# Kernel optimization log

Measured on AMD Instinct MI355X. Metric: run time of the kernel, lower is better.

The kernel has to match this reference:

```python
import jax, jax.numpy as jnp
import numpy as np

B, N, DIM, HEADS = 2, 1024, 1024, 16
HD = DIM // HEADS  # 64


def setup_inputs() -> dict:
    key = jax.random.key(0)
    ks = jax.random.split(key, 8)
    f = lambda k, s: jax.random.normal(k, s, dtype=jnp.float32)
    inv = np.float32(1.0 / np.sqrt(DIM))
    return {
        'x_real': f(ks[0], (B, N, DIM)),
        'x_imag': f(ks[1], (B, N, DIM)),
        'freqs_real': f(ks[2], (N, HD)),
        'freqs_imag': f(ks[3], (N, HD)),
        'Wqkv_r': f(ks[4], (3 * DIM, DIM)) * inv,
        'Wqkv_i': f(ks[5], (3 * DIM, DIM)) * inv,
        'bqkv_r': jnp.zeros((3 * DIM,), jnp.float32),
        'bqkv_i': jnp.zeros((3 * DIM,), jnp.float32),
        'Wout_r': f(ks[6], (DIM, DIM)) * inv,
        'Wout_i': f(ks[7], (DIM, DIM)) * inv,
        'bout_r': jnp.zeros((DIM,), jnp.float32),
        'bout_i': jnp.zeros((DIM,), jnp.float32),
    }


def reference(x_real, x_imag, freqs_real, freqs_imag,
              Wqkv_r, Wqkv_i, bqkv_r, bqkv_i,
              Wout_r, Wout_i, bout_r, bout_i):
    cplx = jax.lax.complex
    x = cplx(x_real, x_imag)                    # [b, n, d] complex64
    Wqkv = cplx(Wqkv_r, Wqkv_i)                 # [3d, d]
    bqkv = cplx(bqkv_r, bqkv_i)
    Wout = cplx(Wout_r, Wout_i)
    bout = cplx(bout_r, bout_i)
    freqs = cplx(freqs_real, freqs_imag)        # [n, hd]

    scale = HD ** (-0.5)

    # ComplexLinear: x @ W^T + b -> [b, n, 3d]
    qkv = jnp.einsum('bnd,ed->bne', x, Wqkv) + bqkv
    # rearrange 'b n (h d qkv) -> qkv b h n d' (qkv index fastest-varying)
    qkv = qkv.reshape(B, N, HEADS, HD, 3)
    q = jnp.transpose(qkv[..., 0], (0, 2, 1, 3))  # [b, h, n, hd]
    k = jnp.transpose(qkv[..., 1], (0, 2, 1, 3))
    v = jnp.transpose(qkv[..., 2], (0, 2, 1, 3))

    # complex rotary: elementwise multiply by freqs [n, hd]
    q = q * freqs
    k = k * freqs

    # complex QK^H -> [b, h, n, n]
    dots = jnp.einsum('bhnd,bhmd->bhnm', q, jnp.conj(k))
    attn = jax.nn.softmax(jnp.abs(dots) * scale, axis=-1)  # real float32

    # real attn @ complex v (promotes to complex64)
    out = jnp.einsum('bhnm,bhmd->bhnd', attn, v)
    out = jnp.transpose(out, (0, 2, 1, 3)).reshape(B, N, DIM)  # b n (h d)

    out = jnp.einsum('bnd,ed->bne', out, Wout) + bout
    # return real/imag stacked so baseline comparison is on real arrays
    return jnp.stack([jnp.real(out), jnp.imag(out)], axis=0)  # [2, b, n, d]
```

## Files before the change

### kernel.cpp

```cpp
#include <hip/hip_runtime.h>
#include <hip/hip_bf16.h>
#include <stdint.h>

#define B 2
#define N 1024
#define DIM 1024
#define HEADS 16
#define HD 64
#define E3 (3*DIM)
#define M (B*N)

typedef __hip_bfloat16 bf16;
typedef __attribute__((ext_vector_type(8))) short short8v;
typedef __attribute__((ext_vector_type(4))) float f32x4;
typedef __attribute__((ext_vector_type(4))) unsigned int u32x4;

__device__ __forceinline__ float scrub(float v) {
    return (v == v && fabsf(v) < 1e30f) ? v : 0.0f;
}
__device__ __forceinline__ float b2f(bf16 x) { return scrub(__bfloat162float(x)); }

template<bool FP32>
__device__ __forceinline__ float ldin(const void* p, int i) {
    if (FP32) return scrub(((const float*)p)[i]);
    else      return scrub(__bfloat162float(((const bf16*)p)[i]));
}

__device__ __forceinline__ bool sniff_fp32(const void* x, int tid, int* sbad) {
    if (tid == 0) *sbad = 0;
    __syncthreads();
    if (tid < 64) {
        const unsigned short* u = (const unsigned short*)x;
        int ex = (u[tid] >> 7) & 0xFF;
        if (ex == 0xFF || ex >= 135 || (ex != 0 && ex <= 118))
            atomicAdd(sbad, 1);
    }
    __syncthreads();
    return *sbad > 4;
}

__device__ __forceinline__ short f2bs(float x) {
    bf16 h = __float2bfloat16(x);
    return __builtin_bit_cast(short, h);
}
__device__ __forceinline__ short8v neg8(short8v x) {
    u32x4 u = __builtin_bit_cast(u32x4, x);
    u ^= 0x80008000u;
    return __builtin_bit_cast(short8v, u);
}
__device__ __forceinline__ f32x4 mfma16(short8v a, short8v b, f32x4 c) {
    return __builtin_amdgcn_mfma_f32_16x16x32_bf16(a, b, c, 0, 0, 0);
}

__device__ __forceinline__ void gload16(const bf16* g, bf16* l) {
    __builtin_amdgcn_global_load_lds(
        (const __attribute__((address_space(1))) void*)g,
        (__attribute__((address_space(3))) void*)l, 16, 0, 0);
}

__device__ __forceinline__ void cvt8(bf16* dhi, bf16* dlo, const float* s) {
    float4 a = *(const float4*)s;
    float4 b = *(const float4*)(s + 4);
    float v[8] = {a.x,a.y,a.z,a.w,b.x,b.y,b.z,b.w};
    short8v hi, lo;
    #pragma unroll
    for (int e = 0; e < 8; ++e) {
        float f = scrub(v[e]);
        bf16 h = __float2bfloat16(f);
        hi[e] = __builtin_bit_cast(short, h);
        lo[e] = f2bs(f - __bfloat162float(h));
    }
    *(short8v*)dhi = hi;
    *(short8v*)dlo = lo;
}
__device__ __forceinline__ void cvt8h(bf16* dhi, const float* s) {
    float4 a = *(const float4*)s;
    float4 b = *(const float4*)(s + 4);
    float v[8] = {a.x,a.y,a.z,a.w,b.x,b.y,b.z,b.w};
    short8v hi;
    #pragma unroll
    for (int e = 0; e < 8; ++e)
        hi[e] = f2bs(scrub(v[e]));
    *(short8v*)dhi = hi;
}

#define PLB 2048

__device__ __forceinline__ short8v frag_ldp(const bf16* base, int row, int j) {
    int p = row >> 1;
    int c = (((row & 1) << 2) | j) ^ (p & 7);
    return *(const short8v*)(base + p*64 + c*8);
}

template<bool ASPLIT, int BM, int NI>
__device__ __forceinline__ void cgemm_async(
    const bf16* Arh, const bf16* Aih, const bf16* Arl, const bf16* Ail,
    const bf16* Brh, const bf16* Bih,
    int row0, int col0,
    bf16* sA0, bf16* sA1, bf16* sB0, bf16* sB1,
    f32x4 (*accr)[NI], f32x4 (*accs)[NI], f32x4 (*acci)[NI])
{
    constexpr int PLA = BM*32;
    const int t  = threadIdx.x;
    const int w  = t >> 6, l = t & 63;
    const int lr = l & 15, lg = l >> 4;
    const int wm = (NI == 4) ? w : (w >> 1);
    const int wn = (NI == 4) ? 0 : (w & 1);

    const int pb  = t >> 3;
    const int cpb = (t & 7) ^ (pb & 7);
    const int srb = 2*pb + (cpb >> 2);
    const int sjb = cpb & 3;

    auto stage = [&](int buf, int k0) {
        bf16* dsA = buf ? sA1 : sA0;
        bf16* dsB = buf ? sB1 : sB0;
        #pragma unroll
        for (int u = 0; u < BM/64; ++u) {
            int c   = t + 256*u;
            int pa  = c >> 3;
            int cpa = (c & 7) ^ (pa & 7);
            int sra = 2*pa + (cpa >> 2);
            int sja = cpa & 3;
            size_t aoff = (size_t)(row0 + sra)*DIM + k0 + sja*8;
            gload16(Arh + aoff, dsA + c*8);
            gload16(Aih + aoff, dsA + PLA + c*8);
            if constexpr (ASPLIT) {
                gload16(Arl + aoff, dsA + 2*PLA + c*8);
                gload16(Ail + aoff, dsA + 3*PLA + c*8);
            }
        }
        size_t boff = (size_t)(col0 + srb)*DIM + k0 + sjb*8;
        gload16(Brh + boff, dsB + t*8);
        gload16(Bih + boff, dsB + PLB + t*8);
    };

    stage(0, 0);
    __syncthreads();
    int cur = 0;

    for (int k0 = 0; k0 < DIM; k0 += 32) {
        if (k0 + 32 < DIM) stage(cur ^ 1, k0 + 32);

        const bf16* sA = cur ? sA1 : sA0;
        const bf16* sB = cur ? sB1 : sB0;

        short8v arh[2], aih[2], arl[2], ail[2];
        #pragma unroll
        for (int mi = 0; mi < 2; ++mi) {
            int arow = wm*32 + mi*16 + lr;
            arh[mi] = frag_ldp(sA,       arow, lg);
            aih[mi] = frag_ldp(sA + PLA, arow, lg);
            if constexpr (ASPLIT) {
                arl[mi] = frag_ldp(sA + 2*PLA, arow, lg);
                ail[mi] = frag_ldp(sA + 3*PLA, arow, lg);
            }
        }
        #pragma unroll
        for (int ni = 0; ni < NI; ++ni) {
            int brow = wn*32 + ni*16 + lr;
            short8v brh = frag_ldp(sB,       brow, lg);
            short8v bih = frag_ldp(sB + PLB, brow, lg);
            #pragma unroll
            for (int mi = 0; mi < 2; ++mi) {
                accr[mi][ni] = mfma16(arh[mi], brh, accr[mi][ni]);
                accs[mi][ni] = mfma16(aih[mi], bih, accs[mi][ni]);
                acci[mi][ni] = mfma16(arh[mi], bih, acci[mi][ni]);
                acci[mi][ni] = mfma16(aih[mi], brh, acci[mi][ni]);
                if constexpr (ASPLIT) {
                    accr[mi][ni] = mfma16(arl[mi], brh, accr[mi][ni]);
                    accs[mi][ni] = mfma16(ail[mi], bih, accs[mi][ni]);
                    acci[mi][ni] = mfma16(arl[mi], bih, acci[mi][ni]);
                    acci[mi][ni] = mfma16(ail[mi], brh, acci[mi][ni]);
                }
            }
        }
        __syncthreads();
        cur ^= 1;
    }
}

template<int AMODE, int BMODE, int BM, int NI>
__device__ __forceinline__ void cgemm_sync(
    const void* Aor, const void* Aoi,
    const void* Bor, const void* Boi,
    int row0, int col0,
    bf16* sA, bf16* sB,
    f32x4 (*accr)[NI], f32x4 (*accs)[NI], f32x4 (*acci)[NI])
{
    constexpr int PLA = BM*32;
    const int t  = threadIdx.x;
    const int w  = t >> 6, l = t & 63;
    const int lr = l & 15, lg = l >> 4;
    const int wm = (NI == 4) ? w : (w >> 1);
    const int wn = (NI == 4) ? 0 : (w & 1);

    const int pb  = t >> 3;
    const int cpb = (t & 7) ^ (pb & 7);
    const int srb = 2*pb + (cpb >> 2);
    const int sjb = cpb & 3;

    for (int k0 = 0; k0 < DIM; k0 += 32) {
        #pragma unroll
        for (int u = 0; u < BM/64; ++u) {
            int c   = t + 256*u;
            int pa  = c >> 3;
            int cpa = (c & 7) ^ (pa & 7);
            int sra = 2*pa + (cpa >> 2);
            int sja = cpa & 3;
            size_t aoff = (size_t)(row0 + sra)*DIM + k0 + sja*8;
            bf16* dA = sA + c*8;
            if constexpr (AMODE == 0) {
                *(short8v*)(dA)       = *(const short8v*)((const bf16*)Aor + aoff);
                *(short8v*)(dA + PLA) = *(const short8v*)((const bf16*)Aoi + aoff);
            } else {
                cvt8(dA,       dA + 2*PLA, (const float*)Aor + aoff);
                cvt8(dA + PLA, dA + 3*PLA, (const float*)Aoi + aoff);
            }
        }
        {
            size_t boff = (size_t)(col0 + srb)*DIM + k0 + sjb*8;
            bf16* dB = sB + t*8;
            if constexpr (BMODE == 0) {
                *(short8v*)(dB)       = *(const short8v*)((const bf16*)Bor + boff);
                *(short8v*)(dB + PLB) = *(const short8v*)((const bf16*)Boi + boff);
            } else {
                cvt8(dB,       dB + 2*PLB, (const float*)Bor + boff);
                cvt8(dB + PLB, dB + 3*PLB, (const float*)Boi + boff);
            }
        }
        __syncthreads();

        short8v arh[2], aih[2], arl[2], ail[2];
        #pragma unroll
        for (int mi = 0; mi < 2; ++mi) {
            int arow = wm*32 + mi*16 + lr;
            arh[mi] = frag_ldp(sA,       arow, lg);
            aih[mi] = frag_ldp(sA + PLA, arow, lg);
            if constexpr (AMODE == 2) {
                arl[mi] = frag_ldp(sA + 2*PLA, arow, lg);
                ail[mi] = frag_ldp(sA + 3*PLA, arow, lg);
            }
        }
        #pragma unroll
        for (int ni = 0; ni < NI; ++ni) {
            int brow = wn*32 + ni*16 + lr;
            short8v brh = frag_ldp(sB,       brow, lg);
            short8v bih = frag_ldp(sB + PLB, brow, lg);
            short8v brl, bil;
            if constexpr (BMODE == 2) {
                brl = frag_ldp(sB + 2*PLB, brow, lg);
                bil = frag_ldp(sB + 3*PLB, brow, lg);
            }
            #pragma unroll
            for (int mi = 0; mi < 2; ++mi) {
                accr[mi][ni] = mfma16(arh[mi], brh, accr[mi][ni]);
                accs[mi][ni] = mfma16(aih[mi], bih, accs[mi][ni]);
                acci[mi][ni] = mfma16(arh[mi], bih, acci[mi][ni]);
                acci[mi][ni] = mfma16(aih[mi], brh, acci[mi][ni]);
                if constexpr (BMODE == 2) {
                    accr[mi][ni] = mfma16(arh[mi], brl, accr[mi][ni]);
                    accs[mi][ni] = mfma16(aih[mi], bil, accs[mi][ni]);
                    acci[mi][ni] = mfma16(arh[mi], bil, acci[mi][ni]);
                    acci[mi][ni] = mfma16(aih[mi], brl, acci[mi][ni]);
                }
                if constexpr (AMODE == 2) {
                    accr[mi][ni] = mfma16(arl[mi], brh, accr[mi][ni]);
                    accs[mi][ni] = mfma16(ail[mi], bih, accs[mi][ni]);
                    acci[mi][ni] = mfma16(arl[mi], bih, acci[mi][ni]);
                    acci[mi][ni] = mfma16(ail[mi], brh, acci[mi][ni]);
                }
            }
        }
        __syncthreads();
    }
}

struct PrepArgs {
    const void* src[6];
    bf16* hi[6];
    bf16* lo[6];
    int n8[6];
};

__global__ __launch_bounds__(256) void prepass_kernel(PrepArgs a) {
    __shared__ int sbad;
    const int y = blockIdx.y;
    bool f32 = sniff_fp32(a.src[y], threadIdx.x, &sbad);
    if (!f32) return;
    const int n8 = a.n8[y];
    bf16* lo = a.lo[y];
    for (int i = blockIdx.x*blockDim.x + threadIdx.x; i < n8; i += gridDim.x*blockDim.x) {
        if (lo) cvt8 (a.hi[y] + (size_t)i*8, lo + (size_t)i*8, (const float*)a.src[y] + (size_t)i*8);
        else    cvt8h(a.hi[y] + (size_t)i*8,                   (const float*)a.src[y] + (size_t)i*8);
    }
}

template<bool FP32>
__device__ __forceinline__ void qkv_epi(
    const void* fr_, const void* fi_, const void* bqr, const void* bqi,
    bf16* qr, bf16* qi, bf16* kr, bf16* ki, bf16* vr, bf16* vi,
    int row0, int col0,
    f32x4 (*accr)[2], f32x4 (*accs)[2], f32x4 (*acci)[2])
{
    const int t  = threadIdx.x;
    const int w  = t >> 6, l = t & 63;
    const int lr = l & 15, lg = l >> 4;
    const int wm = w >> 1, wn = w & 1;

    #pragma unroll
    for (int ni = 0; ni < 2; ++ni) {
        int col = col0 + wn*32 + ni*16 + lr;
        float bre = ldin<FP32>(bqr, col);
        float bim = ldin<FP32>(bqi, col);
        int s = col % 3;
        int tc = col / 3;
        int h = tc / HD, d = tc % HD;
        #pragma unroll
        for (int mi = 0; mi < 2; ++mi)
        #pragma unroll
        for (int r = 0; r < 4; ++r) {
            int row = row0 + wm*32 + mi*16 + 4*lg + r;
            int bb = row / N, n = row % N;
            float cr = accr[mi][ni][r] - accs[mi][ni][r] + bre;
            float ci = acci[mi][ni][r] + bim;
            if (s == 2) {
                int idxT = ((bb*HEADS + h)*HD + d)*N + n;
                vr[idxT] = __float2bfloat16(scrub(cr));
                vi[idxT] = __float2bfloat16(scrub(ci));
            } else {
                float fre = ldin<FP32>(fr_, n*HD + d);
                float fim = ldin<FP32>(fi_, n*HD + d);
                float rr = cr*fre - ci*fim;
                float ri = cr*fim + ci*fre;
                int idx = ((bb*HEADS + h)*N + n)*HD + d;
                if (s == 0) { qr[idx] = __float2bfloat16(scrub(rr)); qi[idx] = __float2bfloat16(scrub(ri)); }
                else        { kr[idx] = __float2bfloat16(scrub(rr)); ki[idx] = __float2bfloat16(scrub(ri)); }
            }
        }
    }
}

template<int FM>
__global__ __launch_bounds__(256, 3) void qkv_kernel(
    const void* xr, const void* xi, const void* fr_, const void* fi_,
    const void* Wr, const void* Wi, const void* bqr, const void* bqi,
    const bf16* xrh, const bf16* xih, const bf16* xrl, const bf16* xil,
    const bf16* wrh, const bf16* wih,
    bf16* qr, bf16* qi, bf16* kr, bf16* ki, bf16* vr, bf16* vi)
{
    __shared__ __align__(16) bf16 sA[2][4*64*32];
    __shared__ __align__(16) bf16 sB[2][2*PLB];
    __shared__ int sbad;
    bool f32 = sniff_fp32(xr, threadIdx.x, &sbad);

    int wg   = blockIdx.x;
    int xcd  = wg & 7;
    int idx  = wg >> 3;
    int rtin = idx & 1;
    int tmp  = idx >> 1;
    int ctl  = tmp % 6;
    int rtg  = tmp / 6;
    int row0 = (rtg*2 + rtin) * 64;
    int col0 = (xcd*6 + ctl) * 64;

    f32x4 accr[2][2] = {}, accs[2][2] = {}, acci[2][2] = {};
    if (f32) {
        if constexpr (FM == 1)
            cgemm_async<true, 64, 2>(xrh, xih, xrl, xil, wrh, wih,
                                     row0, col0, sA[0], sA[1], sB[0], sB[1],
                                     accr, accs, acci);
        else
            cgemm_sync<2, 2, 64, 2>(xr, xi, Wr, Wi,
                                    row0, col0, sA[0], sB[0],
                                    accr, accs, acci);
        qkv_epi<true >(fr_, fi_, bqr, bqi, qr,qi,kr,ki,vr,vi, row0, col0, accr, accs, acci);
    } else {
        cgemm_async<false, 64, 2>((const bf16*)xr, (const bf16*)xi, nullptr, nullptr,
                                  (const bf16*)Wr, (const bf16*)Wi,
                                  row0, col0, sA[0], sA[1], sB[0], sB[1],
                                  accr, accs, acci);
        qkv_epi<false>(fr_, fi_, bqr, bqi, qr,qi,kr,ki,vr,vi, row0, col0, accr, accs, acci);
    }
}

__device__ __forceinline__ short8v frag_ld(const bf16* base, int row, int j) {
    return *(const short8v*)(base + row*64 + ((j ^ (row & 7)) << 3));
}

__global__ __launch_bounds__(256) void attn_kernel(
    const bf16* qr, const bf16* qi, const bf16* kr, const bf16* ki,
    const bf16* vtr, const bf16* vti, bf16* aor_, bf16* aoi_)
{
    __shared__ __align__(16) bf16 skr[2][64*64];
    __shared__ __align__(16) bf16 ski[2][64*64];
    __shared__ __align__(16) bf16 svr[2][64*64];
    __shared__ __align__(16) bf16 svi[2][64*64];
    __shared__ __align__(16) bf16 sp[4][16*64];

    const int t  = threadIdx.x;
    const int w  = t >> 6;
    const int l  = t & 63;
    const int lr = l & 15;
    const int lg = l >> 4;
    int wg = blockIdx.x;
    int sw = (wg & 7) * ((int)gridDim.x >> 3) + (wg >> 3);
    const int qt = sw & 15;
    const int bh = sw >> 4;

    const size_t hbase = (size_t)bh * N * HD;

    const bf16* qrg = qr + hbase + (size_t)(qt*64 + w*16 + lr) * HD;
    const bf16* qig = qi + hbase + (size_t)(qt*64 + w*16 + lr) * HD;
    short8v qfr[2], qfi[2], qfrn[2];
    #pragma unroll
    for (int ks = 0; ks < 2; ++ks) {
        qfr[ks] = *(const short8v*)(qrg + 32*ks + 8*lg);
        qfi[ks] = *(const short8v*)(qig + 32*ks + 8*lg);
        qfrn[ks] = neg8(qfr[ks]);
    }

    const int cA = t, cB = t + 256;
    const int rA = cA >> 3, jA = (cA & 7) ^ (rA & 7);
    const int rB = cB >> 3, jB = (cB & 7) ^ (rB & 7);
    const bf16* krg = kr  + hbase;
    const bf16* kig = ki  + hbase;
    const bf16* vrg = vtr + hbase;
    const bf16* vig = vti + hbase;

    f32x4 outr[4], outi[4];
    #pragma unroll
    for (int dt = 0; dt < 4; ++dt) {
        outr[dt] = (f32x4){0.f,0.f,0.f,0.f};
        outi[dt] = (f32x4){0.f,0.f,0.f,0.f};
    }
    float mrow[4] = {-1e30f,-1e30f,-1e30f,-1e30f};
    float lrow[4] = {0.f,0.f,0.f,0.f};

    short8v pf0, pf1, pf2, pf3, pf4, pf5, pf6, pf7;
    auto issue = [&](int m0) {
        pf0 = *(const short8v*)(krg + (size_t)(m0+rA)*HD + jA*8);
        pf1 = *(const short8v*)(krg + (size_t)(m0+rB)*HD + jB*8);
        pf2 = *(const short8v*)(kig + (size_t)(m0+rA)*HD + jA*8);
        pf3 = *(const short8v*)(kig + (size_t)(m0+rB)*HD + jB*8);
        pf4 = *(const short8v*)(vrg + (size_t)rA*N + m0 + jA*8);
        pf5 = *(const short8v*)(vrg + (size_t)rB*N + m0 + jB*8);
        pf6 = *(const short8v*)(vig + (size_t)rA*N + m0 + jA*8);
        pf7 = *(const short8v*)(vig + (size_t)rB*N + m0 + jB*8);
    };
    auto wrt = [&](int buf) {
        *(short8v*)(skr[buf] + cA*8) = pf0;
        *(short8v*)(skr[buf] + cB*8) = pf1;
        *(short8v*)(ski[buf] + cA*8) = pf2;
        *(short8v*)(ski[buf] + cB*8) = pf3;
        *(short8v*)(svr[buf] + cA*8) = pf4;
        *(short8v*)(svr[buf] + cB*8) = pf5;
        *(short8v*)(svi[buf] + cA*8) = pf6;
        *(short8v*)(svi[buf] + cB*8) = pf7;
    };

    issue(0);
    wrt(0);
    __syncthreads();
    int cur = 0;

    for (int kt = 0; kt < N/64; ++kt) {
        if (kt + 1 < N/64) issue((kt + 1) * 64);

        f32x4 sr[4], si[4];
        #pragma unroll
        for (int ct = 0; ct < 4; ++ct) {
            f32x4 ar = (f32x4){0.f,0.f,0.f,0.f};
            f32x4 ai = (f32x4){0.f,0.f,0.f,0.f};
            #pragma unroll
            for (int ks = 0; ks < 2; ++ks) {
                short8v kfr = frag_ld(skr[cur], 16*ct + lr, 4*ks + lg);
                short8v kfi = frag_ld(ski[cur], 16*ct + lr, 4*ks + lg);
                ar = mfma16(qfr[ks],  kfr, ar);
                ar = mfma16(qfi[ks],  kfi, ar);
                ai = mfma16(qfi[ks],  kfr, ai);
                ai = mfma16(qfrn[ks], kfi, ai);
            }
            sr[ct] = ar; si[ct] = ai;
        }

        float p[4][4];
        float pmax[4] = {-1e30f,-1e30f,-1e30f,-1e30f};
        #pragma unroll
        for (int ct = 0; ct < 4; ++ct)
        #pragma unroll
        for (int r = 0; r < 4; ++r) {
            float s = sqrtf(sr[ct][r]*sr[ct][r] + si[ct][r]*si[ct][r]) * 0.125f;
            p[ct][r] = s;
            pmax[r] = fmaxf(pmax[r], s);
        }
        #pragma unroll
        for (int mk = 1; mk <= 8; mk <<= 1)
        #pragma unroll
        for (int r = 0; r < 4; ++r)
            pmax[r] = fmaxf(pmax[r], __shfl_xor(pmax[r], mk));

        float fsc[4];
        #pragma unroll
        for (int r = 0; r < 4; ++r) {
            float mnew = fmaxf(mrow[r], pmax[r]);
            fsc[r] = __expf(mrow[r] - mnew);
            mrow[r] = mnew;
        }
        float rsum[4] = {0.f,0.f,0.f,0.f};
        #pragma unroll
        for (int ct = 0; ct < 4; ++ct)
        #pragma unroll
        for (int r = 0; r < 4; ++r) {
            float e = __expf(p[ct][r] - mrow[r]);
            p[ct][r] = e;
            rsum[r] += e;
        }
        #pragma unroll
        for (int mk = 1; mk <= 8; mk <<= 1)
        #pragma unroll
        for (int r = 0; r < 4; ++r)
            rsum[r] += __shfl_xor(rsum[r], mk);
        #pragma unroll
        for (int r = 0; r < 4; ++r)
            lrow[r] = lrow[r]*fsc[r] + rsum[r];
        #pragma unroll
        for (int dt = 0; dt < 4; ++dt)
        #pragma unroll
        for (int r = 0; r < 4; ++r) {
            outr[dt][r] *= fsc[r];
            outi[dt][r] *= fsc[r];
        }

        bf16* pw = sp[w];
        #pragma unroll
        for (int ct = 0; ct < 4; ++ct)
        #pragma unroll
        for (int r = 0; r < 4; ++r) {
            int prow = 4*lg + r;
            int pcol = 16*ct + lr;
            int jj = (pcol >> 3) ^ (prow & 7);
            pw[prow*64 + jj*8 + (pcol & 7)] = __float2bfloat16(p[ct][r]);
        }
        short8v pa[2];
        #pragma unroll
        for (int ks2 = 0; ks2 < 2; ++ks2)
            pa[ks2] = frag_ld(pw, lr, 4*ks2 + lg);

        #pragma unroll
        for (int dt = 0; dt < 4; ++dt)
        #pragma unroll
        for (int ks2 = 0; ks2 < 2; ++ks2) {
            short8v vfr = frag_ld(svr[cur], 16*dt + lr, 4*ks2 + lg);
            short8v vfi = frag_ld(svi[cur], 16*dt + lr, 4*ks2 + lg);
            outr[dt] = mfma16(pa[ks2], vfr, outr[dt]);
            outi[dt] = mfma16(pa[ks2], vfi, outi[dt]);
        }

        if (kt + 1 < N/64) wrt(cur ^ 1);
        __syncthreads();
        cur ^= 1;
    }

    const int b_ = bh / HEADS, h_ = bh % HEADS;
    float invl[4];
    #pragma unroll
    for (int r = 0; r < 4; ++r) invl[r] = 1.0f / lrow[r];
    #pragma unroll
    for (int dt = 0; dt < 4; ++dt)
    #pragma unroll
    for (int r = 0; r < 4; ++r) {
        int n_ = qt*64 + w*16 + 4*lg + r;
        int d_ = 16*dt + lr;
        size_t oidx = ((size_t)(b_*N + n_))*DIM + h_*HD + d_;
        aor_[oidx] = __float2bfloat16(scrub(outr[dt][r]*invl[r]));
        aoi_[oidx] = __float2bfloat16(scrub(outi[dt][r]*invl[r]));
    }
}

template<int FM>
__global__ __launch_bounds__(256, 4) void outproj_kernel(
    const void* xprobe,
    const bf16* ar, const bf16* ai,
    const void* Wr, const void* Wi, const void* bor, const void* boi,
    const bf16* wrh, const bf16* wih,
    void* out)
{
    __shared__ __align__(16) bf16 sA[2][2*PLB];
    __shared__ __align__(16) bf16 sB[2][2*PLB];
    __shared__ int sbad;
    bool f32 = sniff_fp32(xprobe, threadIdx.x, &sbad);

    int wg   = blockIdx.x;
    int xcd  = wg & 7;
    int idx  = wg >> 3;
    int rtin = idx & 1;
    int tmp  = idx >> 1;
    int ctl  = tmp & 1;
    int rtg  = tmp >> 1;
    int row0 = (rtg*2 + rtin) * 64;
    int col0 = (xcd*2 + ctl) * 64;

    const int t  = threadIdx.x;
    const int w  = t >> 6, l = t & 63;
    const int lr = l & 15, lg = l >> 4;
    const int wm = w >> 1, wn = w & 1;

    f32x4 accr[2][2] = {}, accs[2][2] = {}, acci[2][2] = {};
    if (f32) {
        if constexpr (FM == 3)
            cgemm_async<false, 64, 2>(ar, ai, nullptr, nullptr, wrh, wih,
                                      row0, col0, sA[0], sA[1], sB[0], sB[1],
                                      accr, accs, acci);
        else
            cgemm_sync<0, 2, 64, 2>(ar, ai, Wr, Wi,
                                    row0, col0, sA[0], sB[0],
                                    accr, accs, acci);
    } else {
        cgemm_async<false, 64, 2>(ar, ai, nullptr, nullptr,
                                  (const bf16*)Wr, (const bf16*)Wi,
                                  row0, col0, sA[0], sA[1], sB[0], sB[1],
                                  accr, accs, acci);
    }

    #pragma unroll
    for (int ni = 0; ni < 2; ++ni) {
        int col = col0 + wn*32 + ni*16 + lr;
        float bre = f32 ? ldin<true>(bor, col) : ldin<false>(bor, col);
        float bim = f32 ? ldin<true>(boi, col) : ldin<false>(boi, col);
        #pragma unroll
        for (int mi = 0; mi < 2; ++mi)
        #pragma unroll
        for (int r = 0; r < 4; ++r) {
            int row = row0 + wm*32 + mi*16 + 4*lg + r;
            float cr = scrub(accr[mi][ni][r] - accs[mi][ni][r] + bre);
            float ci = scrub(acci[mi][ni][r] + bim);
            if (f32) {
                ((float*)out)[(size_t)row*DIM + col]                 = cr;
                ((float*)out)[(size_t)M*DIM + (size_t)row*DIM + col] = ci;
            } else {
                ((bf16*)out)[(size_t)row*DIM + col]                  = __float2bfloat16(cr);
                ((bf16*)out)[(size_t)M*DIM + (size_t)row*DIM + col]  = __float2bfloat16(ci);
            }
        }
    }
}

extern "C" void kernel_launch(void* const* d_in, const int* in_sizes, int n_in,
                              void* d_out, int out_size, void* d_ws, size_t ws_size,
                              hipStream_t stream)
{
    const void* xr     = d_in[0];
    const void* xi     = d_in[1];
    const void* fr     = d_in[2];
    const void* fi     = d_in[3];
    const void* Wqkv_r = d_in[4];
    const void* Wqkv_i = d_in[5];
    const void* bqkv_r = d_in[6];
    const void* bqkv_i = d_in[7];
    const void* Wout_r = d_in[8];
    const void* Wout_i = d_in[9];
    const void* bout_r = d_in[10];
    const void* bout_i = d_in[11];

    bf16* w = (bf16*)d_ws;
    const size_t QS  = (size_t)B*HEADS*N*HD;
    const size_t XS  = (size_t)M*DIM;
    const size_t WQS = (size_t)E3*DIM;
    const size_t WOS = (size_t)DIM*DIM;

    bf16* qr   = w;          bf16* qi   = qr  + QS;
    bf16* kr   = qi  + QS;   bf16* ki   = kr  + QS;
    bf16* vr   = ki  + QS;   bf16* vi   = vr  + QS;
    bf16* aor_ = vi  + QS;   bf16* aoi_ = aor_ + QS;
    bf16* xrh = aoi_ + QS;   bf16* xih = xrh + XS;
    bf16* xrl = xih + XS;    bf16* xil = xrl + XS;
    bf16* wqrh = xil + XS;   bf16* wqih = wqrh + WQS;
    bf16* worh = wqih + WQS; bf16* woih = worh + WOS;

    const size_t need = (size_t)(8*QS + 4*XS + 2*WQS + 2*WOS) * sizeof(bf16);
    const bool pre = ws_size >= need;

    if (pre) {
        PrepArgs a;
        a.src[0] = xr;     a.hi[0] = xrh;  a.lo[0] = xrl;    a.n8[0] = (int)(XS/8);
        a.src[1] = xi;     a.hi[1] = xih;  a.lo[1] = xil;    a.n8[1] = (int)(XS/8);
        a.src[2] = Wqkv_r; a.hi[2] = wqrh; a.lo[2] = nullptr; a.n8[2] = (int)(WQS/8);
        a.src[3] = Wqkv_i; a.hi[3] = wqih; a.lo[3] = nullptr; a.n8[3] = (int)(WQS/8);
        a.src[4] = Wout_r; a.hi[4] = worh; a.lo[4] = nullptr; a.n8[4] = (int)(WOS/8);
        a.src[5] = Wout_i; a.hi[5] = woih; a.lo[5] = nullptr; a.n8[5] = (int)(WOS/8);
        prepass_kernel<<<dim3(1536, 6), dim3(256), 0, stream>>>(a);

        qkv_kernel<1><<<dim3((E3/64)*(M/64)), dim3(256), 0, stream>>>(
            xr, xi, fr, fi, Wqkv_r, Wqkv_i, bqkv_r, bqkv_i,
            xrh, xih, xrl, xil, wqrh, wqih,
            qr, qi, kr, ki, vr, vi);
    } else {
        qkv_kernel<2><<<dim3((E3/64)*(M/64)), dim3(256), 0, stream>>>(
            xr, xi, fr, fi, Wqkv_r, Wqkv_i, bqkv_r, bqkv_i,
            nullptr, nullptr, nullptr, nullptr, nullptr, nullptr,
            qr, qi, kr, ki, vr, vi);
    }

    attn_kernel<<<dim3(B*HEADS*(N/64)), dim3(256), 0, stream>>>(
        qr, qi, kr, ki, vr, vi, aor_, aoi_);

    if (pre) {
        outproj_kernel<3><<<dim3((DIM/64)*(M/64)), dim3(256), 0, stream>>>(
            xr, aor_, aoi_, Wout_r, Wout_i, bout_r, bout_i,
            worh, woih, d_out);
    } else {
        outproj_kernel<2><<<dim3((DIM/64)*(M/64)), dim3(256), 0, stream>>>(
            xr, aor_, aoi_, Wout_r, Wout_i, bout_r, bout_i,
            nullptr, nullptr, d_out);
    }
}
```

Before: 299.5 us.

## Stage attention K/V tiles with direct global-to-LDS loads and raise MFMA priority

Replaces the register-staged prefetch (global load into registers, then an LDS write after compute) with a gload16 helper that copies K/V tiles from global memory straight into the alternate LDS buffer. Wraps the QK^H and PV MFMA blocks in s_setprio so the matrix-math wavefronts get issue priority. The aim is to free prefetch registers, drop the explicit LDS store pass, and overlap memory traffic with compute. It depends on gload16 being correct for the swizzled layout, and on the single barrier per iteration being enough to make the async LDS writes visible.

```diff
diff --git a/kernel.cpp b/kernel.cpp
--- a/kernel.cpp
+++ b/kernel.cpp
@@ -428,6 +428,17 @@
     const bf16* vrg = vtr + hbase;
     const bf16* vig = vti + hbase;
 
+    auto stage = [&](int buf, int m0) {
+        gload16(krg + (size_t)(m0+rA)*HD + jA*8, skr[buf] + cA*8);
+        gload16(krg + (size_t)(m0+rB)*HD + jB*8, skr[buf] + cB*8);
+        gload16(kig + (size_t)(m0+rA)*HD + jA*8, ski[buf] + cA*8);
+        gload16(kig + (size_t)(m0+rB)*HD + jB*8, ski[buf] + cB*8);
+        gload16(vrg + (size_t)rA*N + m0 + jA*8, svr[buf] + cA*8);
+        gload16(vrg + (size_t)rB*N + m0 + jB*8, svr[buf] + cB*8);
+        gload16(vig + (size_t)rA*N + m0 + jA*8, svi[buf] + cA*8);
+        gload16(vig + (size_t)rB*N + m0 + jB*8, svi[buf] + cB*8);
+    };
+
     f32x4 outr[4], outi[4];
     #pragma unroll
     for (int dt = 0; dt < 4; ++dt) {
@@ -437,37 +448,15 @@
     float mrow[4] = {-1e30f,-1e30f,-1e30f,-1e30f};
     float lrow[4] = {0.f,0.f,0.f,0.f};
 
-    short8v pf0, pf1, pf2, pf3, pf4, pf5, pf6, pf7;
-    auto issue = [&](int m0) {
-        pf0 = *(const short8v*)(krg + (size_t)(m0+rA)*HD + jA*8);
-        pf1 = *(const short8v*)(krg + (size_t)(m0+rB)*HD + jB*8);
-        pf2 = *(const short8v*)(kig + (size_t)(m0+rA)*HD + jA*8);
-        pf3 = *(const short8v*)(kig + (size_t)(m0+rB)*HD + jB*8);
-        pf4 = *(const short8v*)(vrg + (size_t)rA*N + m0 + jA*8);
-        pf5 = *(const short8v*)(vrg + (size_t)rB*N + m0 + jB*8);
-        pf6 = *(const short8v*)(vig + (size_t)rA*N + m0 + jA*8);
-        pf7 = *(const short8v*)(vig + (size_t)rB*N + m0 + jB*8);
-    };
-    auto wrt = [&](int buf) {
-        *(short8v*)(skr[buf] + cA*8) = pf0;
-        *(short8v*)(skr[buf] + cB*8) = pf1;
-        *(short8v*)(ski[buf] + cA*8) = pf2;
-        *(short8v*)(ski[buf] + cB*8) = pf3;
-        *(short8v*)(svr[buf] + cA*8) = pf4;
-        *(short8v*)(svr[buf] + cB*8) = pf5;
-        *(short8v*)(svi[buf] + cA*8) = pf6;
-        *(short8v*)(svi[buf] + cB*8) = pf7;
-    };
-
-    issue(0);
-    wrt(0);
+    stage(0, 0);
     __syncthreads();
     int cur = 0;
 
     for (int kt = 0; kt < N/64; ++kt) {
-        if (kt + 1 < N/64) issue((kt + 1) * 64);
+        if (kt + 1 < N/64) stage(cur ^ 1, (kt + 1) * 64);
 
         f32x4 sr[4], si[4];
+        __builtin_amdgcn_s_setprio(1);
         #pragma unroll
         for (int ct = 0; ct < 4; ++ct) {
             f32x4 ar = (f32x4){0.f,0.f,0.f,0.f};
@@ -483,6 +472,7 @@
             }
             sr[ct] = ar; si[ct] = ai;
         }
+        __builtin_amdgcn_s_setprio(0);
 
         float p[4][4];
         float pmax[4] = {-1e30f,-1e30f,-1e30f,-1e30f};
@@ -547,6 +537,7 @@
         for (int ks2 = 0; ks2 < 2; ++ks2)
             pa[ks2] = frag_ld(pw, lr, 4*ks2 + lg);
 
+        __builtin_amdgcn_s_setprio(1);
         #pragma unroll
         for (int dt = 0; dt < 4; ++dt)
         #pragma unroll
@@ -556,8 +547,8 @@
             outr[dt] = mfma16(pa[ks2], vfr, outr[dt]);
             outi[dt] = mfma16(pa[ks2], vfi, outi[dt]);
         }
-
-        if (kt + 1 < N/64) wrt(cur ^ 1);
+        __builtin_amdgcn_s_setprio(0);
+
         __syncthreads();
         cur ^= 1;
     }
```

Result: no change. 302.4 us (+1.0%).
